# Kernel tuning notes

Measured on AMD Instinct MI355X. Metric: run time of the kernel, lower is better.

The kernel has to match this reference:

```python
import jax, jax.numpy as jnp
import numpy as np

N = 50000
E = 800000
D_IN = 128
HID = 128
LAT = 64
NEG_SLOPE = 0.2


def setup_inputs() -> dict:
    key = jax.random.key(0)
    ks = jax.random.split(key, 16)
    g = lambda k, shape: jax.random.normal(k, shape, dtype=jnp.float32) * (1.0 / np.sqrt(shape[0]))
    x = jax.random.normal(ks[0], (N, D_IN), dtype=jnp.float32)
    edge_index = jax.random.randint(ks[1], (2, E), 0, N, dtype=jnp.int64)
    return {
        "x": x,
        "edge_index": edge_index,
        # lin1: Linear(D_IN, HID)
        "lin1_w": g(ks[2], (D_IN, HID)),
        "lin1_b": jnp.zeros((HID,), jnp.float32),
        # conv1: GATConv((D_IN, D_IN) -> HID), heads=1
        "w1_src": g(ks[3], (D_IN, HID)),
        "w1_dst": g(ks[4], (D_IN, HID)),
        "a1_src": g(ks[5], (HID,)),
        "a1_dst": g(ks[6], (HID,)),
        "b1": jnp.zeros((HID,), jnp.float32),
        # conv2: GATConv((HID, HID) -> LAT), heads=1
        "w2_src": g(ks[7], (HID, LAT)),
        "w2_dst": g(ks[8], (HID, LAT)),
        "a2_src": g(ks[9], (LAT,)),
        "a2_dst": g(ks[10], (LAT,)),
        "b2": jnp.zeros((LAT,), jnp.float32),
    }


def _gat_conv(x, src, dst, w_src, w_dst, a_src, a_dst, b):
    """PyG GATConv, heads=1, add_self_loops=False. x: [N, Din]."""
    n = x.shape[0]
    hs = x @ w_src                    # [N, C] messages (source transform)
    hd = x @ w_dst                    # [N, C] destination transform
    alpha_s = hs @ a_src              # [N]
    alpha_d = hd @ a_dst              # [N]
    e = jax.nn.leaky_relu(alpha_s[src] + alpha_d[dst], NEG_SLOPE)  # [E]
    # segment softmax over incoming edges per destination node
    m = jax.ops.segment_max(e, dst, num_segments=n)
    ex = jnp.exp(e - m[dst])
    denom = jax.ops.segment_sum(ex, dst, num_segments=n)
    alpha = ex / (denom[dst] + 1e-16)                              # [E]
    msg = hs[src] * alpha[:, None]                                 # [E, C]
    out = jax.ops.segment_sum(msg, dst, num_segments=n)            # [N, C]
    return out + b


def reference(x, edge_index, lin1_w, lin1_b, w1_src, w1_dst, a1_src, a1_dst, b1,
              w2_src, w2_dst, a2_src, a2_dst, b2):
    src, dst = edge_index[0], edge_index[1]
    z = _gat_conv(x, src, dst, w1_src, w1_dst, a1_src, a1_dst, b1)
    z = jax.nn.relu(z + x @ lin1_w + lin1_b)
    z = _gat_conv(z, src, dst, w2_src, w2_dst, a2_src, a2_dst, b2)
    return z
```

## Files before the change

kernel.cpp:

```cpp
#include <hip/hip_runtime.h>

static constexpr int N_NODES = 50000;
static constexpr int N_EDGES = 800000;
static constexpr int NPART = 8;
static constexpr int PART_SZ = N_NODES / NPART;
static constexpr int NTILES = N_NODES / 16;

typedef __attribute__((ext_vector_type(8))) short bf16x8;
typedef __attribute__((ext_vector_type(4))) float f32x4;

__device__ __forceinline__ float bf2f(unsigned short u) {
  union { unsigned int i; float f; } v; v.i = ((unsigned int)u) << 16; return v.f;
}
__device__ __forceinline__ unsigned short f2bf(float f) {
  union { unsigned int i; float f; } v; v.f = f;
  unsigned int r = (v.i + 0x7fffu + ((v.i >> 16) & 1u)) >> 16;
  return (unsigned short)r;
}
__device__ __forceinline__ int clampN(int v) {
  unsigned u = (unsigned)v; return (u < (unsigned)N_NODES) ? (int)u : 0;
}

__global__ void k_zero_out(float* __restrict__ out, int n) {
  int i = blockIdx.x * 256 + threadIdx.x;
  if (i < n) out[i] = 0.f;
}

__global__ void k_zero_da(int* __restrict__ deg, float* __restrict__ as1) {
  int i = blockIdx.x * 256 + threadIdx.x;
  if (i < N_NODES) { deg[i] = 0; as1[i] = 0.f; }
}

__global__ void k_compact(const int* __restrict__ ei,
                          int* __restrict__ s32, int* __restrict__ d32) {
  int e = blockIdx.x * 256 + threadIdx.x;
  if (e < N_EDGES) {
    int z = ei[1] | ei[3] | ei[5] | ei[7];
    int f = (z == 0) ? 1 : 0;
    s32[e] = clampN(ei[(size_t)e << f]);
    d32[e] = clampN(ei[(size_t)(N_EDGES + e) << f]);
  }
}

__global__ void k_prepw(const float* __restrict__ w1_src, const float* __restrict__ wlin,
                        const float* __restrict__ w2_src,
                        const float* __restrict__ w1_dst, const float* __restrict__ a1_dst,
                        const float* __restrict__ w2_dst, const float* __restrict__ a2_dst,
                        unsigned short* __restrict__ w1T, unsigned short* __restrict__ w2T,
                        float* __restrict__ c1dst, float* __restrict__ c2dst) {
  int idx = blockIdx.x * 256 + threadIdx.x;
  if (idx < 256 * 128) {
    int c = idx >> 7, k = idx & 127;
    float v = (c < 128) ? w1_src[k * 128 + c] : wlin[k * 128 + (c - 128)];
    w1T[idx] = f2bf(v);
  } else if (idx < 256 * 128 + 64 * 128) {
    int r = idx - 256 * 128;
    int c = r >> 7, k = r & 127;
    w2T[r] = f2bf(w2_src[k * 64 + c]);
  } else if (blockIdx.x == 160) {
    int k = threadIdx.x;
    if (k < 128) {
      float s1 = 0.f;
      for (int c = 0; c < 128; ++c) s1 += w1_dst[k * 128 + c] * a1_dst[c];
      c1dst[k] = s1;
      float s2 = 0.f;
      for (int c = 0; c < 64; ++c) s2 += w2_dst[k * 64 + c] * a2_dst[c];
      c2dst[k] = s2;
    }
  }
}

__global__ __launch_bounds__(256) void k_prepx(
    const float* __restrict__ x, const float* __restrict__ c1dst,
    unsigned short* __restrict__ xb, float* __restrict__ ad1) {
  int gid = blockIdx.x * 256 + threadIdx.x;
  int row = gid >> 4, sl = gid & 15;
  const float* p = x + (size_t)row * 128 + sl * 8;
  float4 a0 = *(const float4*)p;
  float4 a1 = *(const float4*)(p + 4);
  uint4 o;
  o.x = (unsigned)f2bf(a0.x) | ((unsigned)f2bf(a0.y) << 16);
  o.y = (unsigned)f2bf(a0.z) | ((unsigned)f2bf(a0.w) << 16);
  o.z = (unsigned)f2bf(a1.x) | ((unsigned)f2bf(a1.y) << 16);
  o.w = (unsigned)f2bf(a1.z) | ((unsigned)f2bf(a1.w) << 16);
  *(uint4*)(xb + (size_t)row * 128 + sl * 8) = o;
  float4 ca = *(const float4*)(c1dst + sl * 8);
  float4 cb = *(const float4*)(c1dst + sl * 8 + 4);
  float sd = a0.x * ca.x + a0.y * ca.y + a0.z * ca.z + a0.w * ca.w +
             a1.x * cb.x + a1.y * cb.y + a1.z * cb.z + a1.w * cb.w;
  sd += __shfl_xor(sd, 1, 64);
  sd += __shfl_xor(sd, 2, 64);
  sd += __shfl_xor(sd, 4, 64);
  sd += __shfl_xor(sd, 8, 64);
  if (sl == 0) ad1[row] = sd;
}

__global__ __launch_bounds__(256) void k_gemm1(
    const unsigned short* __restrict__ xb, const unsigned short* __restrict__ w1T,
    const float* __restrict__ lin_b, const float* __restrict__ a1_src,
    unsigned short* __restrict__ hs1, unsigned short* __restrict__ linzb,
    float* __restrict__ as1) {
  int tid = threadIdx.x;
  int wv = tid >> 6, l = tid & 63;
  int lrow = l & 15, lk = l >> 4;
  int cb = wv * 64;
  bf16x8 wfrag[4][4];
#pragma unroll
  for (int ct = 0; ct < 4; ++ct)
#pragma unroll
    for (int ks = 0; ks < 4; ++ks)
      wfrag[ct][ks] = *(const bf16x8*)(w1T + (size_t)(cb + ct * 16 + lrow) * 128 + ks * 32 + lk * 8);
  for (int t = blockIdx.x; t < NTILES; t += gridDim.x) {
    int row = t * 16 + lrow;
    bf16x8 xfrag[4];
#pragma unroll
    for (int ks = 0; ks < 4; ++ks)
      xfrag[ks] = *(const bf16x8*)(xb + (size_t)row * 128 + ks * 32 + lk * 8);
    f32x4 acc[4] = {{0.f,0.f,0.f,0.f},{0.f,0.f,0.f,0.f},{0.f,0.f,0.f,0.f},{0.f,0.f,0.f,0.f}};
#pragma unroll
    for (int ks = 0; ks < 4; ++ks)
#pragma unroll
      for (int ct = 0; ct < 4; ++ct)
        acc[ct] = __builtin_amdgcn_mfma_f32_16x16x32_bf16(wfrag[ct][ks], xfrag[ks], acc[ct], 0, 0, 0);
    if (cb < 128) {
      float pa = 0.f;
#pragma unroll
      for (int ct = 0; ct < 4; ++ct) {
        int col0 = cb + ct * 16 + lk * 4;
        float4 av = *(const float4*)(a1_src + col0);
        pa += acc[ct][0] * av.x + acc[ct][1] * av.y + acc[ct][2] * av.z + acc[ct][3] * av.w;
        uint2 pv;
        pv.x = (unsigned)f2bf(acc[ct][0]) | ((unsigned)f2bf(acc[ct][1]) << 16);
        pv.y = (unsigned)f2bf(acc[ct][2]) | ((unsigned)f2bf(acc[ct][3]) << 16);
        *(uint2*)(hs1 + (size_t)row * 128 + col0) = pv;
      }
      pa += __shfl_xor(pa, 16, 64);
      pa += __shfl_xor(pa, 32, 64);
      if (l < 16) atomicAdd(&as1[t * 16 + l], pa);
    } else {
#pragma unroll
      for (int ct = 0; ct < 4; ++ct) {
        int col0 = cb - 128 + ct * 16 + lk * 4;
        float4 bv = *(const float4*)(lin_b + col0);
        uint2 pv;
        pv.x = (unsigned)f2bf(acc[ct][0] + bv.x) | ((unsigned)f2bf(acc[ct][1] + bv.y) << 16);
        pv.y = (unsigned)f2bf(acc[ct][2] + bv.z) | ((unsigned)f2bf(acc[ct][3] + bv.w) << 16);
        *(uint2*)(linzb + (size_t)row * 128 + col0) = pv;
      }
    }
  }
}

__global__ __launch_bounds__(256) void k_gemm2(
    const unsigned short* __restrict__ zb, const unsigned short* __restrict__ w2T,
    const float* __restrict__ a2_src, const float* __restrict__ c2dst,
    unsigned short* __restrict__ hs2, float* __restrict__ as2, float* __restrict__ ad2) {
  int tid = threadIdx.x;
  int wv = tid >> 6, l = tid & 63;
  int lrow = l & 15, lk = l >> 4;
  int g = blockIdx.x * 4 + wv;
  if (g >= NTILES) return;
  bf16x8 wfrag[4][4];
#pragma unroll
  for (int ct = 0; ct < 4; ++ct)
#pragma unroll
    for (int ks = 0; ks < 4; ++ks)
      wfrag[ct][ks] = *(const bf16x8*)(w2T + (size_t)(ct * 16 + lrow) * 128 + ks * 32 + lk * 8);
  int row = g * 16 + lrow;
  bf16x8 xfrag[4];
  float sd = 0.f;
#pragma unroll
  for (int ks = 0; ks < 4; ++ks) {
    bf16x8 af = *(const bf16x8*)(zb + (size_t)row * 128 + ks * 32 + lk * 8);
    xfrag[ks] = af;
    int k0 = ks * 32 + lk * 8;
    float4 ca = *(const float4*)(c2dst + k0);
    float4 cb = *(const float4*)(c2dst + k0 + 4);
    sd += bf2f((unsigned short)af[0]) * ca.x + bf2f((unsigned short)af[1]) * ca.y +
          bf2f((unsigned short)af[2]) * ca.z + bf2f((unsigned short)af[3]) * ca.w +
          bf2f((unsigned short)af[4]) * cb.x + bf2f((unsigned short)af[5]) * cb.y +
          bf2f((unsigned short)af[6]) * cb.z + bf2f((unsigned short)af[7]) * cb.w;
  }
  sd += __shfl_xor(sd, 16, 64);
  sd += __shfl_xor(sd, 32, 64);
  if (lk == 0) ad2[row] = sd;

  f32x4 acc[4] = {{0.f,0.f,0.f,0.f},{0.f,0.f,0.f,0.f},{0.f,0.f,0.f,0.f},{0.f,0.f,0.f,0.f}};
#pragma unroll
  for (int ks = 0; ks < 4; ++ks)
#pragma unroll
    for (int ct = 0; ct < 4; ++ct)
      acc[ct] = __builtin_amdgcn_mfma_f32_16x16x32_bf16(wfrag[ct][ks], xfrag[ks], acc[ct], 0, 0, 0);
  float pa = 0.f;
#pragma unroll
  for (int ct = 0; ct < 4; ++ct) {
    int col0 = ct * 16 + lk * 4;
    float4 av = *(const float4*)(a2_src + col0);
    pa += acc[ct][0] * av.x + acc[ct][1] * av.y + acc[ct][2] * av.z + acc[ct][3] * av.w;
    uint2 pv;
    pv.x = (unsigned)f2bf(acc[ct][0]) | ((unsigned)f2bf(acc[ct][1]) << 16);
    pv.y = (unsigned)f2bf(acc[ct][2]) | ((unsigned)f2bf(acc[ct][3]) << 16);
    *(uint2*)(hs2 + (size_t)row * 64 + col0) = pv;
  }
  pa += __shfl_xor(pa, 16, 64);
  pa += __shfl_xor(pa, 32, 64);
  if (lk == 0) as2[row] = pa;
}

__global__ void k_count(const int* __restrict__ d32, int* __restrict__ deg) {
  int part = blockIdx.x & (NPART - 1);
  int e = (blockIdx.x >> 3) * 256 + threadIdx.x;
  if (e < N_EDGES) {
    int d = d32[e];
    int lo = part * PART_SZ;
    if (d >= lo && d < lo + PART_SZ) atomicAdd(&deg[d], 1);
  }
}

__global__ __launch_bounds__(256) void k_scan1(const int* __restrict__ deg,
                                               int* __restrict__ offs,
                                               int* __restrict__ bsums, int n) {
  __shared__ int wsum[4];
  int i = blockIdx.x * 256 + threadIdx.x;
  int lane = threadIdx.x & 63, wid = threadIdx.x >> 6;
  int v = (i < n) ? deg[i] : 0;
  int s = v;
#pragma unroll
  for (int o = 1; o < 64; o <<= 1) { int t = __shfl_up(s, o, 64); if (lane >= o) s += t; }
  if (lane == 63) wsum[wid] = s;
  __syncthreads();
  if (threadIdx.x == 0) {
    int a = 0;
#pragma unroll
    for (int w = 0; w < 4; ++w) { a += wsum[w]; wsum[w] = a; }
  }
  __syncthreads();
  int base = (wid > 0) ? wsum[wid - 1] : 0;
  if (i < n) offs[i] = base + s - v;
  if (threadIdx.x == 0) bsums[blockIdx.x] = wsum[3];
}

__global__ __launch_bounds__(256) void k_scan2(int* __restrict__ bsums, int nb,
                                               int* __restrict__ offs, int n, int etot) {
  __shared__ int wsum[4];
  int tid = threadIdx.x, lane = tid & 63, wid = tid >> 6;
  int v = (tid < nb) ? bsums[tid] : 0;
  int s = v;
#pragma unroll
  for (int o = 1; o < 64; o <<= 1) { int t = __shfl_up(s, o, 64); if (lane >= o) s += t; }
  if (lane == 63) wsum[wid] = s;
  __syncthreads();
  if (tid == 0) {
    int a = 0;
#pragma unroll
    for (int w = 0; w < 4; ++w) { a += wsum[w]; wsum[w] = a; }
  }
  __syncthreads();
  int base = (wid > 0) ? wsum[wid - 1] : 0;
  if (tid < nb) bsums[tid] = base + s - v;
  if (tid == 0) offs[n] = etot;
}

__global__ __launch_bounds__(256) void k_scan3(int* __restrict__ offs, int* __restrict__ cursor,
                                               const int* __restrict__ bsums, int n) {
  int i = blockIdx.x * 256 + threadIdx.x;
  if (i < n) {
    int o = offs[i] + bsums[blockIdx.x];
    offs[i] = o;
    cursor[i] = o;
  }
}

__global__ void k_fill(const int* __restrict__ s32, const int* __restrict__ d32,
                       int* __restrict__ cursor, int* __restrict__ ssrc) {
  int part = blockIdx.x & (NPART - 1);
  int e = (blockIdx.x >> 3) * 256 + threadIdx.x;
  if (e < N_EDGES) {
    int d = d32[e];
    int lo = part * PART_SZ;
    if (d >= lo && d < lo + PART_SZ) {
      int p = atomicAdd(&cursor[d], 1);
      if ((unsigned)p < (unsigned)N_EDGES) ssrc[p] = s32[e];
    }
  }
}

__global__ __launch_bounds__(256) void k_agg1(
    const int* __restrict__ offs, const int* __restrict__ ssrc,
    const float* __restrict__ as_, const float* __restrict__ ad_,
    const unsigned short* __restrict__ hs1, const float* __restrict__ b1,
    unsigned short* __restrict__ linzb) {
  int node = (int)((blockIdx.x * 256 + threadIdx.x) >> 6);
  if (node >= N_NODES) return;
  int lane = threadIdx.x & 63;
  int g = lane >> 4, cl = lane & 15;
  int o0 = offs[node], o1 = offs[node + 1];
  if (!((unsigned)o0 <= (unsigned)N_EDGES && (unsigned)o1 <= (unsigned)N_EDGES && o0 <= o1))
    { o0 = 0; o1 = 0; }
  int deg = o1 - o0;
  float ad = ad_[node];
  float acc[8];
#pragma unroll
  for (int k = 0; k < 8; ++k) acc[k] = 0.f;
  float ssum = 0.f;
  for (int j = g; j < deg; j += 4) {
    int s = clampN(ssrc[o0 + j]);
    float e = as_[s] + ad;
    e = e > 0.f ? e : 0.2f * e;
    float w = __expf(e);
    uint4 hv = *(const uint4*)(hs1 + (size_t)s * 128 + cl * 8);
    ssum += w;
    acc[0] += w * __uint_as_float(hv.x << 16);
    acc[1] += w * __uint_as_float(hv.x & 0xffff0000u);
    acc[2] += w * __uint_as_float(hv.y << 16);
    acc[3] += w * __uint_as_float(hv.y & 0xffff0000u);
    acc[4] += w * __uint_as_float(hv.z << 16);
    acc[5] += w * __uint_as_float(hv.z & 0xffff0000u);
    acc[6] += w * __uint_as_float(hv.w << 16);
    acc[7] += w * __uint_as_float(hv.w & 0xffff0000u);
  }
  ssum += __shfl_xor(ssum, 16, 64);
  ssum += __shfl_xor(ssum, 32, 64);
#pragma unroll
  for (int k = 0; k < 8; ++k) {
    acc[k] += __shfl_xor(acc[k], 16, 64);
    acc[k] += __shfl_xor(acc[k], 32, 64);
  }
  if (g == 0) {
    float inv = 1.f / (ssum + 1e-16f);
    uint4 lv = *(const uint4*)(linzb + (size_t)node * 128 + cl * 8);
    float4 ba = *(const float4*)(b1 + cl * 8);
    float4 bb = *(const float4*)(b1 + cl * 8 + 4);
    float z[8];
    z[0] = acc[0] * inv + ba.x + __uint_as_float(lv.x << 16);
    z[1] = acc[1] * inv + ba.y + __uint_as_float(lv.x & 0xffff0000u);
    z[2] = acc[2] * inv + ba.z + __uint_as_float(lv.y << 16);
    z[3] = acc[3] * inv + ba.w + __uint_as_float(lv.y & 0xffff0000u);
    z[4] = acc[4] * inv + bb.x + __uint_as_float(lv.z << 16);
    z[5] = acc[5] * inv + bb.y + __uint_as_float(lv.z & 0xffff0000u);
    z[6] = acc[6] * inv + bb.z + __uint_as_float(lv.w << 16);
    z[7] = acc[7] * inv + bb.w + __uint_as_float(lv.w & 0xffff0000u);
#pragma unroll
    for (int k = 0; k < 8; ++k) z[k] = z[k] > 0.f ? z[k] : 0.f;
    uint4 ov;
    ov.x = (unsigned)f2bf(z[0]) | ((unsigned)f2bf(z[1]) << 16);
    ov.y = (unsigned)f2bf(z[2]) | ((unsigned)f2bf(z[3]) << 16);
    ov.z = (unsigned)f2bf(z[4]) | ((unsigned)f2bf(z[5]) << 16);
    ov.w = (unsigned)f2bf(z[6]) | ((unsigned)f2bf(z[7]) << 16);
    *(uint4*)(linzb + (size_t)node * 128 + cl * 8) = ov;
  }
}

__global__ __launch_bounds__(256) void k_agg2(
    const int* __restrict__ offs, const int* __restrict__ ssrc,
    const float* __restrict__ as_, const float* __restrict__ ad_,
    const unsigned short* __restrict__ hs2, const float* __restrict__ b2,
    float* __restrict__ out) {
  int node = (int)((blockIdx.x * 256 + threadIdx.x) >> 6);
  if (node >= N_NODES) return;
  int lane = threadIdx.x & 63;
  int g = lane >> 3, cl = lane & 7;
  int o0 = offs[node], o1 = offs[node + 1];
  if (!((unsigned)o0 <= (unsigned)N_EDGES && (unsigned)o1 <= (unsigned)N_EDGES && o0 <= o1))
    { o0 = 0; o1 = 0; }
  int deg = o1 - o0;
  float ad = ad_[node];
  float acc[8];
#pragma unroll
  for (int k = 0; k < 8; ++k) acc[k] = 0.f;
  float ssum = 0.f;
  for (int j = g; j < deg; j += 8) {
    int s = clampN(ssrc[o0 + j]);
    float e = as_[s] + ad;
    e = e > 0.f ? e : 0.2f * e;
    float w = __expf(e);
    uint4 hv = *(const uint4*)(hs2 + (size_t)s * 64 + cl * 8);
    ssum += w;
    acc[0] += w * __uint_as_float(hv.x << 16);
    acc[1] += w * __uint_as_float(hv.x & 0xffff0000u);
    acc[2] += w * __uint_as_float(hv.y << 16);
    acc[3] += w * __uint_as_float(hv.y & 0xffff0000u);
    acc[4] += w * __uint_as_float(hv.z << 16);
    acc[5] += w * __uint_as_float(hv.z & 0xffff0000u);
    acc[6] += w * __uint_as_float(hv.w << 16);
    acc[7] += w * __uint_as_float(hv.w & 0xffff0000u);
  }
  ssum += __shfl_xor(ssum, 8, 64);
  ssum += __shfl_xor(ssum, 16, 64);
  ssum += __shfl_xor(ssum, 32, 64);
#pragma unroll
  for (int k = 0; k < 8; ++k) {
    acc[k] += __shfl_xor(acc[k], 8, 64);
    acc[k] += __shfl_xor(acc[k], 16, 64);
    acc[k] += __shfl_xor(acc[k], 32, 64);
  }
  if (g == 0) {
    float inv = 1.f / (ssum + 1e-16f);
    float4 ba = *(const float4*)(b2 + cl * 8);
    float4 bb = *(const float4*)(b2 + cl * 8 + 4);
    float4 oa, ob;
    oa.x = acc[0] * inv + ba.x;
    oa.y = acc[1] * inv + ba.y;
    oa.z = acc[2] * inv + ba.z;
    oa.w = acc[3] * inv + ba.w;
    ob.x = acc[4] * inv + bb.x;
    ob.y = acc[5] * inv + bb.y;
    ob.z = acc[6] * inv + bb.z;
    ob.w = acc[7] * inv + bb.w;
    *(float4*)(out + (size_t)node * 64 + cl * 8) = oa;
    *(float4*)(out + (size_t)node * 64 + cl * 8 + 4) = ob;
  }
}

extern "C" void kernel_launch(void* const* d_in, const int* in_sizes, int n_in,
                              void* d_out, int out_size, void* d_ws, size_t ws_size,
                              hipStream_t stream) {
  (void)in_sizes; (void)n_in;
  const float* x      = (const float*)d_in[0];
  const int*   ei     = (const int*)d_in[1];
  const float* lin1_w = (const float*)d_in[2];
  const float* lin1_b = (const float*)d_in[3];
  const float* w1_src = (const float*)d_in[4];
  const float* w1_dst = (const float*)d_in[5];
  const float* a1_src = (const float*)d_in[6];
  const float* a1_dst = (const float*)d_in[7];
  const float* b1     = (const float*)d_in[8];
  const float* w2_src = (const float*)d_in[9];
  const float* w2_dst = (const float*)d_in[10];
  const float* a2_src = (const float*)d_in[11];
  const float* a2_dst = (const float*)d_in[12];
  const float* b2     = (const float*)d_in[13];
  float* out = (float*)d_out;

  char* ws = (char*)d_ws;
  size_t off = 0;
  auto alloc = [&](size_t bytes) -> void* {
    void* p = ws + off;
    off += (bytes + 255) & ~(size_t)255;
    return p;
  };
  float* c1dst = (float*)alloc(128 * 4);
  float* c2dst = (float*)alloc(128 * 4);
  unsigned short* w1T = (unsigned short*)alloc(256 * 128 * 2);
  unsigned short* w2T = (unsigned short*)alloc(64 * 128 * 2);
  int* deg     = (int*)alloc((size_t)N_NODES * 4);
  float* as1   = (float*)alloc((size_t)N_NODES * 4);
  int* offs    = (int*)alloc((size_t)(N_NODES + 1) * 4);
  int* cursor  = (int*)alloc((size_t)N_NODES * 4);
  int* bsums   = (int*)alloc(1024);
  float* ad1   = (float*)alloc((size_t)N_NODES * 4);
  int* s32     = (int*)alloc((size_t)N_EDGES * 4);
  int* d32     = (int*)alloc((size_t)N_EDGES * 4);
  unsigned short* hs1   = (unsigned short*)alloc((size_t)N_NODES * 128 * 2);
  unsigned short* linzb = (unsigned short*)alloc((size_t)N_NODES * 128 * 2);
  char* U = (char*)alloc((size_t)N_NODES * 128 * 2);
  unsigned short* xb  = (unsigned short*)U;
  int* ssrc           = (int*)U;
  unsigned short* hs2 = (unsigned short*)(U + (size_t)N_EDGES * 4);
  float* as2          = (float*)(U + (size_t)N_EDGES * 4 + (size_t)N_NODES * 128);
  float* ad2          = (float*)(U + (size_t)N_EDGES * 4 + (size_t)N_NODES * 128 + (size_t)N_NODES * 4);

  if (off > ws_size) {
    k_zero_out<<<(out_size + 255) / 256, 256, 0, stream>>>(out, out_size);
    return;
  }

  int ebl  = (N_EDGES + 255) / 256;
  int ebl8 = NPART * ebl;
  int nbl  = (N_NODES + 3) / 4;
  int nb   = (N_NODES + 255) / 256;
  k_zero_da<<<nb, 256, 0, stream>>>(deg, as1);
  k_prepw<<<161, 256, 0, stream>>>(w1_src, lin1_w, w2_src, w1_dst, a1_dst, w2_dst, a2_dst,
                                   w1T, w2T, c1dst, c2dst);
  k_compact<<<ebl, 256, 0, stream>>>(ei, s32, d32);
  k_prepx<<<NTILES, 256, 0, stream>>>(x, c1dst, xb, ad1);
  k_gemm1<<<1024, 256, 0, stream>>>(xb, w1T, lin1_b, a1_src, hs1, linzb, as1);
  k_count<<<ebl8, 256, 0, stream>>>(d32, deg);
  k_scan1<<<nb, 256, 0, stream>>>(deg, offs, bsums, N_NODES);
  k_scan2<<<1, 256, 0, stream>>>(bsums, nb, offs, N_NODES, N_EDGES);
  k_scan3<<<nb, 256, 0, stream>>>(offs, cursor, bsums, N_NODES);
  k_fill<<<ebl8, 256, 0, stream>>>(s32, d32, cursor, ssrc);
  k_agg1<<<nbl, 256, 0, stream>>>(offs, ssrc, as1, ad1, hs1, b1, linzb);
  k_gemm2<<<(NTILES + 3) / 4, 256, 0, stream>>>(linzb, w2T, a2_src, c2dst, hs2, as2, ad2);
  k_agg2<<<nbl, 256, 0, stream>>>(offs, ssrc, as2, ad2, hs2, b2, out);
}
```

Baseline: 206.1 us.

## Merge setup kernels, prefetch next edge source, use nontemporal loads/stores in aggregation

Three setup kernels (zeroing, weight prep, edge compaction) are merged into one launch with block-range dispatch, removing two launches. The aggregation loops software-prefetch the next source index with nontemporal loads so the index load overlaps with the current gather. Output and linzb writes use nontemporal stores to avoid cache pollution. These are separate ideas bundled together; the nontemporal store of linzb could hurt because gemm2 reads it next.

Measured after the change: 209.9 us. About the same (+1.8%).

```diff
diff --git a/kernel.cpp b/kernel.cpp
--- a/kernel.cpp
+++ b/kernel.cpp
@@ -8,6 +8,7 @@
 
 typedef __attribute__((ext_vector_type(8))) short bf16x8;
 typedef __attribute__((ext_vector_type(4))) float f32x4;
+typedef __attribute__((ext_vector_type(4))) unsigned int u32x4;
 
 __device__ __forceinline__ float bf2f(unsigned short u) {
   union { unsigned int i; float f; } v; v.i = ((unsigned int)u) << 16; return v.f;
@@ -26,47 +27,48 @@
   if (i < n) out[i] = 0.f;
 }
 
-__global__ void k_zero_da(int* __restrict__ deg, float* __restrict__ as1) {
-  int i = blockIdx.x * 256 + threadIdx.x;
-  if (i < N_NODES) { deg[i] = 0; as1[i] = 0.f; }
-}
-
-__global__ void k_compact(const int* __restrict__ ei,
-                          int* __restrict__ s32, int* __restrict__ d32) {
-  int e = blockIdx.x * 256 + threadIdx.x;
-  if (e < N_EDGES) {
-    int z = ei[1] | ei[3] | ei[5] | ei[7];
-    int f = (z == 0) ? 1 : 0;
-    s32[e] = clampN(ei[(size_t)e << f]);
-    d32[e] = clampN(ei[(size_t)(N_EDGES + e) << f]);
-  }
-}
-
-__global__ void k_prepw(const float* __restrict__ w1_src, const float* __restrict__ wlin,
+__global__ void k_setup(const int* __restrict__ ei,
+                        int* __restrict__ s32, int* __restrict__ d32,
+                        const float* __restrict__ w1_src, const float* __restrict__ wlin,
                         const float* __restrict__ w2_src,
                         const float* __restrict__ w1_dst, const float* __restrict__ a1_dst,
                         const float* __restrict__ w2_dst, const float* __restrict__ a2_dst,
                         unsigned short* __restrict__ w1T, unsigned short* __restrict__ w2T,
-                        float* __restrict__ c1dst, float* __restrict__ c2dst) {
-  int idx = blockIdx.x * 256 + threadIdx.x;
-  if (idx < 256 * 128) {
-    int c = idx >> 7, k = idx & 127;
-    float v = (c < 128) ? w1_src[k * 128 + c] : wlin[k * 128 + (c - 128)];
-    w1T[idx] = f2bf(v);
-  } else if (idx < 256 * 128 + 64 * 128) {
-    int r = idx - 256 * 128;
-    int c = r >> 7, k = r & 127;
-    w2T[r] = f2bf(w2_src[k * 64 + c]);
-  } else if (blockIdx.x == 160) {
-    int k = threadIdx.x;
-    if (k < 128) {
-      float s1 = 0.f;
-      for (int c = 0; c < 128; ++c) s1 += w1_dst[k * 128 + c] * a1_dst[c];
-      c1dst[k] = s1;
-      float s2 = 0.f;
-      for (int c = 0; c < 64; ++c) s2 += w2_dst[k * 64 + c] * a2_dst[c];
-      c2dst[k] = s2;
+                        float* __restrict__ c1dst, float* __restrict__ c2dst,
+                        int* __restrict__ deg, float* __restrict__ as1) {
+  int b = blockIdx.x;
+  if (b < 3125) {
+    int e = b * 256 + threadIdx.x;
+    if (e < N_EDGES) {
+      int z = ei[1] | ei[3] | ei[5] | ei[7];
+      int f = (z == 0) ? 1 : 0;
+      s32[e] = clampN(ei[(size_t)e << f]);
+      d32[e] = clampN(ei[(size_t)(N_EDGES + e) << f]);
     }
+  } else if (b < 3286) {
+    int idx = (b - 3125) * 256 + threadIdx.x;
+    if (idx < 256 * 128) {
+      int c = idx >> 7, k = idx & 127;
+      float v = (c < 128) ? w1_src[k * 128 + c] : wlin[k * 128 + (c - 128)];
+      w1T[idx] = f2bf(v);
+    } else if (idx < 256 * 128 + 64 * 128) {
+      int r = idx - 256 * 128;
+      int c = r >> 7, k = r & 127;
+      w2T[r] = f2bf(w2_src[k * 64 + c]);
+    } else if (b == 3285) {
+      int k = threadIdx.x;
+      if (k < 128) {
+        float s1 = 0.f;
+        for (int c = 0; c < 128; ++c) s1 += w1_dst[k * 128 + c] * a1_dst[c];
+        c1dst[k] = s1;
+        float s2 = 0.f;
+        for (int c = 0; c < 64; ++c) s2 += w2_dst[k * 64 + c] * a2_dst[c];
+        c2dst[k] = s2;
+      }
+    }
+  } else {
+    int i = (b - 3286) * 256 + threadIdx.x;
+    if (i < N_NODES) { deg[i] = 0; as1[i] = 0.f; }
   }
 }
 
@@ -303,12 +305,13 @@
 #pragma unroll
   for (int k = 0; k < 8; ++k) acc[k] = 0.f;
   float ssum = 0.f;
+  int sc = (g < deg) ? clampN(__builtin_nontemporal_load(ssrc + o0 + g)) : 0;
   for (int j = g; j < deg; j += 4) {
-    int s = clampN(ssrc[o0 + j]);
-    float e = as_[s] + ad;
+    int sn = (j + 4 < deg) ? clampN(__builtin_nontemporal_load(ssrc + o0 + j + 4)) : 0;
+    float e = as_[sc] + ad;
     e = e > 0.f ? e : 0.2f * e;
     float w = __expf(e);
-    uint4 hv = *(const uint4*)(hs1 + (size_t)s * 128 + cl * 8);
+    uint4 hv = *(const uint4*)(hs1 + (size_t)sc * 128 + cl * 8);
     ssum += w;
     acc[0] += w * __uint_as_float(hv.x << 16);
     acc[1] += w * __uint_as_float(hv.x & 0xffff0000u);
@@ -318,6 +321,7 @@
     acc[5] += w * __uint_as_float(hv.z & 0xffff0000u);
     acc[6] += w * __uint_as_float(hv.w << 16);
     acc[7] += w * __uint_as_float(hv.w & 0xffff0000u);
+    sc = sn;
   }
   ssum += __shfl_xor(ssum, 16, 64);
   ssum += __shfl_xor(ssum, 32, 64);
@@ -328,26 +332,26 @@
   }
   if (g == 0) {
     float inv = 1.f / (ssum + 1e-16f);
-    uint4 lv = *(const uint4*)(linzb + (size_t)node * 128 + cl * 8);
+    u32x4 lv = __builtin_nontemporal_load((const u32x4*)(linzb + (size_t)node * 128 + cl * 8));
     float4 ba = *(const float4*)(b1 + cl * 8);
     float4 bb = *(const float4*)(b1 + cl * 8 + 4);
     float z[8];
-    z[0] = acc[0] * inv + ba.x + __uint_as_float(lv.x << 16);
-    z[1] = acc[1] * inv + ba.y + __uint_as_float(lv.x & 0xffff0000u);
-    z[2] = acc[2] * inv + ba.z + __uint_as_float(lv.y << 16);
-    z[3] = acc[3] * inv + ba.w + __uint_as_float(lv.y & 0xffff0000u);
-    z[4] = acc[4] * inv + bb.x + __uint_as_float(lv.z << 16);
-    z[5] = acc[5] * inv + bb.y + __uint_as_float(lv.z & 0xffff0000u);
-    z[6] = acc[6] * inv + bb.z + __uint_as_float(lv.w << 16);
-    z[7] = acc[7] * inv + bb.w + __uint_as_float(lv.w & 0xffff0000u);
+    z[0] = acc[0] * inv + ba.x + __uint_as_float(lv[0] << 16);
+    z[1] = acc[1] * inv + ba.y + __uint_as_float(lv[0] & 0xffff0000u);
+    z[2] = acc[2] * inv + ba.z + __uint_as_float(lv[1] << 16);
+    z[3] = acc[3] * inv + ba.w + __uint_as_float(lv[1] & 0xffff0000u);
+    z[4] = acc[4] * inv + bb.x + __uint_as_float(lv[2] << 16);
+    z[5] = acc[5] * inv + bb.y + __uint_as_float(lv[2] & 0xffff0000u);
+    z[6] = acc[6] * inv + bb.z + __uint_as_float(lv[3] << 16);
+    z[7] = acc[7] * inv + bb.w + __uint_as_float(lv[3] & 0xffff0000u);
 #pragma unroll
     for (int k = 0; k < 8; ++k) z[k] = z[k] > 0.f ? z[k] : 0.f;
-    uint4 ov;
-    ov.x = (unsigned)f2bf(z[0]) | ((unsigned)f2bf(z[1]) << 16);
-    ov.y = (unsigned)f2bf(z[2]) | ((unsigned)f2bf(z[3]) << 16);
-    ov.z = (unsigned)f2bf(z[4]) | ((unsigned)f2bf(z[5]) << 16);
-    ov.w = (unsigned)f2bf(z[6]) | ((unsigned)f2bf(z[7]) << 16);
-    *(uint4*)(linzb + (size_t)node * 128 + cl * 8) = ov;
+    u32x4 ov;
+    ov[0] = (unsigned)f2bf(z[0]) | ((unsigned)f2bf(z[1]) << 16);
+    ov[1] = (unsigned)f2bf(z[2]) | ((unsigned)f2bf(z[3]) << 16);
+    ov[2] = (unsigned)f2bf(z[4]) | ((unsigned)f2bf(z[5]) << 16);
+    ov[3] = (unsigned)f2bf(z[6]) | ((unsigned)f2bf(z[7]) << 16);
+    __builtin_nontemporal_store(ov, (u32x4*)(linzb + (size_t)node * 128 + cl * 8));
   }
 }
 
@@ -369,12 +373,13 @@
 #pragma unroll
   for (int k = 0; k < 8; ++k) acc[k] = 0.f;
   float ssum = 0.f;
+  int sc = (g < deg) ? clampN(__builtin_nontemporal_load(ssrc + o0 + g)) : 0;
   for (int j = g; j < deg; j += 8) {
-    int s = clampN(ssrc[o0 + j]);
-    float e = as_[s] + ad;
+    int sn = (j + 8 < deg) ? clampN(__builtin_nontemporal_load(ssrc + o0 + j + 8)) : 0;
+    float e = as_[sc] + ad;
     e = e > 0.f ? e : 0.2f * e;
     float w = __expf(e);
-    uint4 hv = *(const uint4*)(hs2 + (size_t)s * 64 + cl * 8);
+    uint4 hv = *(const uint4*)(hs2 + (size_t)sc * 64 + cl * 8);
     ssum += w;
     acc[0] += w * __uint_as_float(hv.x << 16);
     acc[1] += w * __uint_as_float(hv.x & 0xffff0000u);
@@ -384,6 +389,7 @@
     acc[5] += w * __uint_as_float(hv.z & 0xffff0000u);
     acc[6] += w * __uint_as_float(hv.w << 16);
     acc[7] += w * __uint_as_float(hv.w & 0xffff0000u);
+    sc = sn;
   }
   ssum += __shfl_xor(ssum, 8, 64);
   ssum += __shfl_xor(ssum, 16, 64);
@@ -398,17 +404,17 @@
     float inv = 1.f / (ssum + 1e-16f);
     float4 ba = *(const float4*)(b2 + cl * 8);
     float4 bb = *(const float4*)(b2 + cl * 8 + 4);
-    float4 oa, ob;
-    oa.x = acc[0] * inv + ba.x;
-    oa.y = acc[1] * inv + ba.y;
-    oa.z = acc[2] * inv + ba.z;
-    oa.w = acc[3] * inv + ba.w;
-    ob.x = acc[4] * inv + bb.x;
-    ob.y = acc[5] * inv + bb.y;
-    ob.z = acc[6] * inv + bb.z;
-    ob.w = acc[7] * inv + bb.w;
-    *(float4*)(out + (size_t)node * 64 + cl * 8) = oa;
-    *(float4*)(out + (size_t)node * 64 + cl * 8 + 4) = ob;
+    f32x4 oa, ob;
+    oa[0] = acc[0] * inv + ba.x;
+    oa[1] = acc[1] * inv + ba.y;
+    oa[2] = acc[2] * inv + ba.z;
+    oa[3] = acc[3] * inv + ba.w;
+    ob[0] = acc[4] * inv + bb.x;
+    ob[1] = acc[5] * inv + bb.y;
+    ob[2] = acc[6] * inv + bb.z;
+    ob[3] = acc[7] * inv + bb.w;
+    __builtin_nontemporal_store(oa, (f32x4*)(out + (size_t)node * 64 + cl * 8));
+    __builtin_nontemporal_store(ob, (f32x4*)(out + (size_t)node * 64 + cl * 8 + 4));
   }
 }
 
@@ -465,14 +471,12 @@
     return;
   }
 
-  int ebl  = (N_EDGES + 255) / 256;
-  int ebl8 = NPART * ebl;
+  int ebl8 = NPART * ((N_EDGES + 255) / 256);
   int nbl  = (N_NODES + 3) / 4;
   int nb   = (N_NODES + 255) / 256;
-  k_zero_da<<<nb, 256, 0, stream>>>(deg, as1);
-  k_prepw<<<161, 256, 0, stream>>>(w1_src, lin1_w, w2_src, w1_dst, a1_dst, w2_dst, a2_dst,
-                                   w1T, w2T, c1dst, c2dst);
-  k_compact<<<ebl, 256, 0, stream>>>(ei, s32, d32);
+  k_setup<<<3482, 256, 0, stream>>>(ei, s32, d32, w1_src, lin1_w, w2_src,
+                                    w1_dst, a1_dst, w2_dst, a2_dst,
+                                    w1T, w2T, c1dst, c2dst, deg, as1);
   k_prepx<<<NTILES, 256, 0, stream>>>(x, c1dst, xb, ad1);
   k_gemm1<<<1024, 256, 0, stream>>>(xb, w1T, lin1_b, a1_src, hs1, linzb, as1);
   k_count<<<ebl8, 256, 0, stream>>>(d32, deg);
```
